# Kernel optimization log

Hardware: AMD Instinct MI355X
Metric: run time of the kernel (lower is better)

The kernel has to match this reference:

```python
import jax, jax.numpy as jnp
import numpy as np

# static config (matches init_kwargs and a standard 4-level FPN for ~800px input)
SPATIAL_SHAPES = ((100, 100), (50, 50), (25, 25), (13, 13))  # (H_l, W_l)
B, C, H, L, P = 2, 256, 8, 4, 4
DFFN = 2048
DH = C // H
LQ = sum(h * w for h, w in SPATIAL_SHAPES)  # 13294


def layer_norm(x, g, b, eps=1e-5):
    m = jnp.mean(x, -1, keepdims=True)
    v = jnp.mean((x - m) ** 2, -1, keepdims=True)
    return (x - m) * jax.lax.rsqrt(v + eps) * g + b


def ms_deform_sample(value, loc, attn):
    # value [B,Lv,H,DH], loc [B,Lq,H,L,P,2] in [0,1], attn [B,Lq,H,L,P]
    value = jnp.transpose(value, (0, 2, 1, 3))  # [B,H,Lv,DH]
    lq = loc.shape[1]
    out = jnp.zeros((B, H, lq, DH), value.dtype)
    start = 0
    for l, (Hl, Wl) in enumerate(SPATIAL_SHAPES):
        v = jax.lax.dynamic_slice_in_dim(value, start, Hl * Wl, axis=2)  # [B,H,N_l,DH]
        # grid_sample(align_corners=False) coords: x = loc_x*W - 0.5
        gx = jnp.transpose(loc[:, :, :, l, :, 0], (0, 2, 1, 3)) * Wl - 0.5  # [B,H,Lq,P]
        gy = jnp.transpose(loc[:, :, :, l, :, 1], (0, 2, 1, 3)) * Hl - 0.5
        aw = jnp.transpose(attn[:, :, :, l, :], (0, 2, 1, 3))  # [B,H,Lq,P]
        x0 = jnp.floor(gx)
        y0 = jnp.floor(gy)
        for dx in (0.0, 1.0):
            for dy in (0.0, 1.0):
                xi = x0 + dx
                yi = y0 + dy
                w = (1.0 - jnp.abs(gx - xi)) * (1.0 - jnp.abs(gy - yi))
                valid = (xi >= 0) & (xi < Wl) & (yi >= 0) & (yi < Hl)
                idx = (jnp.clip(yi, 0, Hl - 1) * Wl + jnp.clip(xi, 0, Wl - 1)).astype(jnp.int32)
                g = jnp.take_along_axis(v, idx.reshape(B, H, -1)[..., None], axis=2)  # [B,H,Lq*P,DH]
                ww = (w * aw * valid.astype(w.dtype))[..., None]  # [B,H,Lq,P,1]
                out = out + jnp.sum(g.reshape(B, H, lq, P, DH) * ww, axis=3)
        start += Hl * Wl
    return jnp.transpose(out, (0, 2, 1, 3)).reshape(B, lq, C)


def setup_inputs() -> dict:
    key = jax.random.key(0)
    ks = jax.random.split(key, 16)
    s = 0.02
    return {
        "src": jax.random.normal(ks[0], (B, LQ, C), jnp.float32),
        "pos": jax.random.normal(ks[1], (B, LQ, C), jnp.float32),
        "reference_points": jax.random.uniform(ks[2], (B, LQ, L, 2), jnp.float32),
        "w_value": jax.random.normal(ks[3], (C, C), jnp.float32) * s,
        "b_value": jnp.zeros((C,), jnp.float32),
        "w_off": jax.random.normal(ks[4], (C, H * L * P * 2), jnp.float32) * s,
        "b_off": jax.random.normal(ks[5], (H * L * P * 2,), jnp.float32) * s,
        "w_attn": jax.random.normal(ks[6], (C, H * L * P), jnp.float32) * s,
        "b_attn": jnp.zeros((H * L * P,), jnp.float32),
        "w_out": jax.random.normal(ks[7], (C, C), jnp.float32) * s,
        "b_out": jnp.zeros((C,), jnp.float32),
        "ln1_g": jnp.ones((C,), jnp.float32),
        "ln1_b": jnp.zeros((C,), jnp.float32),
        "w_ffn1": jax.random.normal(ks[8], (C, DFFN), jnp.float32) * s,
        "b_ffn1": jnp.zeros((DFFN,), jnp.float32),
        "w_ffn2": jax.random.normal(ks[9], (DFFN, C), jnp.float32) * s,
        "b_ffn2": jnp.zeros((C,), jnp.float32),
        "ln2_g": jnp.ones((C,), jnp.float32),
        "ln2_b": jnp.zeros((C,), jnp.float32),
    }


def reference(src, pos, reference_points, w_value, b_value, w_off, b_off, w_attn, b_attn,
              w_out, b_out, ln1_g, ln1_b, w_ffn1, b_ffn1, w_ffn2, b_ffn2, ln2_g, ln2_b):
    # DeformableTransformerEncoderLayer.forward (eval mode, no dropout)
    q = src + pos  # with_pos_embed
    lq = q.shape[1]
    value = (src @ w_value + b_value).reshape(B, -1, H, DH)
    off = (q @ w_off + b_off).reshape(B, lq, H, L, P, 2)
    attn = (q @ w_attn + b_attn).reshape(B, lq, H, L * P)
    attn = jax.nn.softmax(attn, axis=-1).reshape(B, lq, H, L, P)
    # offset_normalizer = (W_l, H_l)
    norm = jnp.array([[w, h] for h, w in SPATIAL_SHAPES], dtype=src.dtype)
    loc = reference_points[:, :, None, :, None, :] + off / norm[None, None, None, :, None, :]
    src2 = ms_deform_sample(value, loc, attn) @ w_out + b_out
    x = layer_norm(src + src2, ln1_g, ln1_b)
    ff = jax.nn.relu(x @ w_ffn1 + b_ffn1) @ w_ffn2 + b_ffn2
    return layer_norm(x + ff, ln2_g, ln2_b)
```

## Files before the change

### kernel.cpp

```cpp
#include <hip/hip_runtime.h>

#define LQN   13294
#define NBAT  2
#define MROWS (NBAT * LQN)
#define CCH   256
#define NHEAD 8
#define DHEAD 32
#define NLVL  4
#define NPT   4
#define DFF   2048

typedef short short8 __attribute__((ext_vector_type(8)));
typedef float f32x4 __attribute__((ext_vector_type(4)));
typedef unsigned short u16;
typedef u16 u16x4 __attribute__((ext_vector_type(4)));
typedef unsigned int u32;
typedef u32 u32x4 __attribute__((ext_vector_type(4)));

__device__ __forceinline__ u16 f2bf(float f) {
  unsigned int u = __builtin_bit_cast(unsigned int, f);
  u += 0x7fffu + ((u >> 16) & 1u);
  return (u16)(u >> 16);
}
__device__ __forceinline__ float bf2f(u16 s) {
  unsigned int u = ((unsigned int)s) << 16;
  return __builtin_bit_cast(float, u);
}
__device__ __forceinline__ void async16(const void* g, void* l) {
  __builtin_amdgcn_global_load_lds(
      (const __attribute__((address_space(1))) void*)g,
      (__attribute__((address_space(3))) void*)l, 16, 0, 0);
}

__global__ __launch_bounds__(256, 2)
void gemm_dual(const u16* __restrict__ A0, const u16* __restrict__ BT0,
               const float* __restrict__ bias0, u16* __restrict__ C0,
               const u16* __restrict__ A1, const u16* __restrict__ BT1,
               const float* __restrict__ bias1, u16* __restrict__ C1)
{
  __shared__ u16 As[2][128 * 64];
  __shared__ u16 Bs[2][128 * 64];
  const int t    = threadIdx.x;
  const int lane = t & 63;
  const int wid  = t >> 6;
  const int wm   = wid >> 1, wn = wid & 1;
  const int bm   = blockIdx.x;
  const int bnG  = blockIdx.y;
  const bool first = bnG < 2;
  const u16* A    = first ? A0 : A1;
  const u16* BT   = first ? BT0 : BT1;
  const float* bias = first ? bias0 : bias1;
  const int  bn   = first ? bnG : bnG - 2;
  const int l15  = lane & 15;
  const int kq   = lane >> 4;

  f32x4 acc[4][4];
#pragma unroll
  for (int m = 0; m < 4; ++m)
#pragma unroll
    for (int n = 0; n < 4; ++n) acc[m][n] = (f32x4)0.0f;

  auto stage = [&](int buf, int kt) {
#pragma unroll
    for (int i = 0; i < 4; ++i) {
      const int c   = i * 256 + t;
      const int row = c >> 3;
      const int kg  = (c & 7) ^ (row & 7);
      int ar = bm * 128 + row; ar = ar < MROWS ? ar : MROWS - 1;
      async16(&A[(size_t)ar * 256 + kt + kg * 8], &As[buf][c * 8]);
      const int br = bn * 128 + row;
      async16(&BT[(size_t)br * 256 + kt + kg * 8], &Bs[buf][c * 8]);
    }
  };

  stage(0, 0);
  __syncthreads();
  int cur = 0;

  for (int kt = 0; kt < 256; kt += 64) {
    if (kt + 64 < 256) stage(cur ^ 1, kt + 64);

#pragma unroll
    for (int kk = 0; kk < 2; ++kk) {
      short8 af[4], bfr[4];
#pragma unroll
      for (int m = 0; m < 4; ++m) {
        const int row = wm * 64 + m * 16 + l15;
        const int xb  = (kk * 64 + kq * 16) ^ ((row & 7) << 4);
        af[m] = *(const short8*)((const char*)&As[cur][0] + row * 128 + xb);
      }
#pragma unroll
      for (int n = 0; n < 4; ++n) {
        const int col = wn * 64 + n * 16 + l15;
        const int xb  = (kk * 64 + kq * 16) ^ ((col & 7) << 4);
        bfr[n] = *(const short8*)((const char*)&Bs[cur][0] + col * 128 + xb);
      }
#pragma unroll
      for (int m = 0; m < 4; ++m)
#pragma unroll
        for (int n = 0; n < 4; ++n)
          acc[m][n] = __builtin_amdgcn_mfma_f32_16x16x32_bf16(af[m], bfr[n], acc[m][n], 0, 0, 0);
    }

    __syncthreads();
    cur ^= 1;
  }

  const int crow0 = bm * 128 + wm * 64;
  const int ccol0 = bn * 128 + wn * 64;
#pragma unroll
  for (int n = 0; n < 4; ++n) {
    int col = ccol0 + n * 16 + l15;
    float bv = bias[col];
#pragma unroll
    for (int m = 0; m < 4; ++m) {
      int rbase = crow0 + m * 16 + kq * 4;
#pragma unroll
      for (int j = 0; j < 4; ++j) {
        int row = rbase + j;
        if (row < MROWS) {
          float v = acc[m][n][j] + bv;
          if (first) C0[(size_t)row * 256 + col] = f2bf(v);
          else       C1[(size_t)row * 384 + col] = f2bf(v);
        }
      }
    }
  }
}

__global__ __launch_bounds__(512, 2)
void outproj_ln1(const u16* __restrict__ src2_bf, const u16* __restrict__ WT_out,
                 const float* __restrict__ b_out, const float* __restrict__ src,
                 const float* __restrict__ g1, const float* __restrict__ be1,
                 u16* __restrict__ x_bf)
{
  extern __shared__ char smem[];
  char* As = smem;
  char* Bs = smem + 16384;
  float2* red = (float2*)(smem + 49152);

  const int t    = threadIdx.x;
  const int lane = t & 63;
  const int wid  = t >> 6;
  const int wm   = wid >> 2, wn = wid & 3;
  const int l15  = lane & 15;
  const int kq   = lane >> 4;
  const int bm   = blockIdx.x;

  auto stage = [&](int kt) {
#pragma unroll
    for (int i = 0; i < 2; ++i) {
      const int c   = i * 512 + t;
      const int row = c >> 3;
      const int kg  = (c & 7) ^ (row & 7);
      int ar = bm * 128 + row; ar = ar < MROWS ? ar : MROWS - 1;
      async16(&src2_bf[(size_t)ar * 256 + kt + kg * 8], As + c * 16);
    }
#pragma unroll
    for (int i = 0; i < 4; ++i) {
      const int c   = i * 512 + t;
      const int row = c >> 3;
      const int kg  = (c & 7) ^ (row & 7);
      async16(&WT_out[(size_t)row * 256 + kt + kg * 8], Bs + c * 16);
    }
  };

  f32x4 acc[4][4];
#pragma unroll
  for (int m = 0; m < 4; ++m)
#pragma unroll
    for (int n = 0; n < 4; ++n) acc[m][n] = (f32x4)0.0f;

  for (int kt = 0; kt < 256; kt += 64) {
    stage(kt);
    __syncthreads();

#pragma unroll
    for (int kk = 0; kk < 2; ++kk) {
      short8 af[4], bfr[4];
#pragma unroll
      for (int m = 0; m < 4; ++m) {
        const int row = wm * 64 + m * 16 + l15;
        const int xb  = (kk * 64 + kq * 16) ^ ((row & 7) << 4);
        af[m] = *(const short8*)(As + row * 128 + xb);
      }
#pragma unroll
      for (int n = 0; n < 4; ++n) {
        const int col = wn * 64 + n * 16 + l15;
        const int xb  = (kk * 64 + kq * 16) ^ ((col & 7) << 4);
        bfr[n] = *(const short8*)(Bs + col * 128 + xb);
      }
#pragma unroll
      for (int m = 0; m < 4; ++m)
#pragma unroll
        for (int n = 0; n < 4; ++n)
          acc[m][n] = __builtin_amdgcn_mfma_f32_16x16x32_bf16(af[m], bfr[n], acc[m][n], 0, 0, 0);
    }
    __syncthreads();
  }

#pragma unroll
  for (int n = 0; n < 4; ++n) {
    const int col = wn * 64 + n * 16 + l15;
    const float bv = b_out[col];
#pragma unroll
    for (int m = 0; m < 4; ++m)
#pragma unroll
      for (int j = 0; j < 4; ++j) {
        int row = bm * 128 + wm * 64 + m * 16 + kq * 4 + j;
        row = row < MROWS ? row : MROWS - 1;
        acc[m][n][j] += bv + src[(size_t)row * 256 + col];
      }
  }
  float s1[4][4], s2[4][4];
#pragma unroll
  for (int m = 0; m < 4; ++m)
#pragma unroll
    for (int j = 0; j < 4; ++j) {
      float a = 0.f, b = 0.f;
#pragma unroll
      for (int n = 0; n < 4; ++n) { const float v = acc[m][n][j]; a += v; b += v * v; }
      s1[m][j] = a; s2[m][j] = b;
    }
#pragma unroll
  for (int o = 1; o < 16; o <<= 1)
#pragma unroll
    for (int m = 0; m < 4; ++m)
#pragma unroll
      for (int j = 0; j < 4; ++j) {
        s1[m][j] += __shfl_xor(s1[m][j], o, 64);
        s2[m][j] += __shfl_xor(s2[m][j], o, 64);
      }
  if (l15 == 0)
#pragma unroll
    for (int m = 0; m < 4; ++m)
#pragma unroll
      for (int j = 0; j < 4; ++j)
        red[(wm * 64 + m * 16 + kq * 4 + j) * 4 + wn] = make_float2(s1[m][j], s2[m][j]);
  __syncthreads();
  float mean[4][4], rstd[4][4];
#pragma unroll
  for (int m = 0; m < 4; ++m)
#pragma unroll
    for (int j = 0; j < 4; ++j) {
      const int rl = wm * 64 + m * 16 + kq * 4 + j;
      float a = 0.f, b = 0.f;
#pragma unroll
      for (int w = 0; w < 4; ++w) { const float2 r = red[rl * 4 + w]; a += r.x; b += r.y; }
      const float mu = a * (1.0f / 256.0f);
      mean[m][j] = mu;
      rstd[m][j] = rsqrtf(b * (1.0f / 256.0f) - mu * mu + 1e-5f);
    }
#pragma unroll
  for (int n = 0; n < 4; ++n) {
    const int col = wn * 64 + n * 16 + l15;
    const float gg = g1[col], bb = be1[col];
#pragma unroll
    for (int m = 0; m < 4; ++m)
#pragma unroll
      for (int j = 0; j < 4; ++j) {
        const int row = bm * 128 + wm * 64 + m * 16 + kq * 4 + j;
        if (row < MROWS) {
          const float y = (acc[m][n][j] - mean[m][j]) * rstd[m][j] * gg + bb;
          x_bf[(size_t)row * 256 + col] = f2bf(y);
        }
      }
  }
}

__global__ __launch_bounds__(1024, 2)
void ffn_ln2(const u16* __restrict__ x_bf, const u16* __restrict__ W1T,
             const u16* __restrict__ W2T, const float* __restrict__ b1,
             const float* __restrict__ b2,
             const float* __restrict__ g2, const float* __restrict__ be2,
             float* __restrict__ out)
{
  extern __shared__ char smem[];
  u16*  w1s = (u16*)(smem);
  u16*  w2s = (u16*)(smem + 65536);
  char* ps  = smem + 131072;
  float2* red = (float2*)(smem + 149504);

  const int t    = threadIdx.x;
  const int lane = t & 63;
  const int wid  = t >> 6;
  const int l15  = lane & 15;
  const int kq   = lane >> 4;
  const int bm   = blockIdx.x;
  const int pwm  = wid >> 1, pwn = wid & 1;
  const int vwm  = wid >> 2, vwn = wid & 3;

  short8 xr[8];
  {
    int ar = bm * 128 + pwm * 16 + l15;
    ar = ar < MROWS ? ar : MROWS - 1;
    const char* xb = (const char*)x_bf + (size_t)ar * 512 + kq * 16;
#pragma unroll
    for (int ks = 0; ks < 8; ++ks) xr[ks] = *(const short8*)(xb + ks * 64);
  }

  auto stage = [&](int buf, int it) {
#pragma unroll
    for (int i = 0; i < 2; ++i) {
      const int c  = i * 1024 + t;
      const int r1 = c >> 5;
      const int k1 = ((c & 31) ^ (r1 & 7)) * 8;
      async16(&W1T[(size_t)(it * 64 + r1) * 256 + k1], &w1s[buf * 16384 + c * 8]);
      const int r2 = c >> 3;
      const int k2 = ((c & 7) ^ (r2 & 7)) * 8;
      async16(&W2T[(size_t)r2 * 2048 + it * 64 + k2], &w2s[buf * 16384 + c * 8]);
    }
  };

  f32x4 acc[2][4];
#pragma unroll
  for (int m = 0; m < 2; ++m)
#pragma unroll
    for (int n = 0; n < 4; ++n) acc[m][n] = (f32x4)0.0f;

  stage(0, 0);
  __syncthreads();

  for (int it = 0; it < 32; ++it) {
    const int cur = it & 1;
    if (it < 31) stage(cur ^ 1, it + 1);

    f32x4 p[2];
    p[0] = (f32x4)0.0f; p[1] = (f32x4)0.0f;
#pragma unroll
    for (int ks = 0; ks < 8; ++ks) {
#pragma unroll
      for (int n = 0; n < 2; ++n) {
        const int wrow = pwn * 32 + n * 16 + l15;
        const int xb   = (((ks * 4 + kq) ^ (wrow & 7)) << 4);
        const short8 bfr = *(const short8*)((const char*)&w1s[cur * 16384] + wrow * 512 + xb);
        p[n] = __builtin_amdgcn_mfma_f32_16x16x32_bf16(xr[ks], bfr, p[n], 0, 0, 0);
      }
    }

#pragma unroll
    for (int n = 0; n < 2; ++n) {
      const int col = pwn * 32 + n * 16 + l15;
      const float bv = b1[it * 64 + col];
#pragma unroll
      for (int j = 0; j < 4; ++j) {
        const int prow = pwm * 16 + kq * 4 + j;
        *(u16*)(ps + prow * 144 + col * 2) = f2bf(fmaxf(p[n][j] + bv, 0.0f));
      }
    }
    __syncthreads();

#pragma unroll
    for (int kk = 0; kk < 2; ++kk) {
      short8 paf[2];
#pragma unroll
      for (int m = 0; m < 2; ++m) {
        const int arow = vwm * 32 + m * 16 + l15;
        paf[m] = *(const short8*)(ps + arow * 144 + (kk * 4 + kq) * 16);
      }
#pragma unroll
      for (int n = 0; n < 4; ++n) {
        const int brow = vwn * 64 + n * 16 + l15;
        const int xb   = (((kk * 4 + kq) ^ (brow & 7)) << 4);
        const short8 bfr = *(const short8*)((const char*)&w2s[cur * 16384] + brow * 128 + xb);
#pragma unroll
        for (int m = 0; m < 2; ++m)
          acc[m][n] = __builtin_amdgcn_mfma_f32_16x16x32_bf16(paf[m], bfr, acc[m][n], 0, 0, 0);
      }
    }
    __syncthreads();
  }

#pragma unroll
  for (int n = 0; n < 4; ++n) {
    const int col = vwn * 64 + n * 16 + l15;
    const float bv = b2[col];
#pragma unroll
    for (int m = 0; m < 2; ++m)
#pragma unroll
      for (int j = 0; j < 4; ++j) {
        int row = bm * 128 + vwm * 32 + m * 16 + kq * 4 + j;
        row = row < MROWS ? row : MROWS - 1;
        acc[m][n][j] += bv + bf2f(x_bf[(size_t)row * 256 + col]);
      }
  }
  float s1[2][4], s2[2][4];
#pragma unroll
  for (int m = 0; m < 2; ++m)
#pragma unroll
    for (int j = 0; j < 4; ++j) {
      float a = 0.f, b = 0.f;
#pragma unroll
      for (int n = 0; n < 4; ++n) { const float v = acc[m][n][j]; a += v; b += v * v; }
      s1[m][j] = a; s2[m][j] = b;
    }
#pragma unroll
  for (int o = 1; o < 16; o <<= 1)
#pragma unroll
    for (int m = 0; m < 2; ++m)
#pragma unroll
      for (int j = 0; j < 4; ++j) {
        s1[m][j] += __shfl_xor(s1[m][j], o, 64);
        s2[m][j] += __shfl_xor(s2[m][j], o, 64);
      }
  if (l15 == 0)
#pragma unroll
    for (int m = 0; m < 2; ++m)
#pragma unroll
      for (int j = 0; j < 4; ++j)
        red[(vwm * 32 + m * 16 + kq * 4 + j) * 4 + vwn] = make_float2(s1[m][j], s2[m][j]);
  __syncthreads();
  float mean[2][4], rstd[2][4];
#pragma unroll
  for (int m = 0; m < 2; ++m)
#pragma unroll
    for (int j = 0; j < 4; ++j) {
      const int rl = vwm * 32 + m * 16 + kq * 4 + j;
      float a = 0.f, b = 0.f;
#pragma unroll
      for (int w = 0; w < 4; ++w) { const float2 r = red[rl * 4 + w]; a += r.x; b += r.y; }
      const float mu = a * (1.0f / 256.0f);
      mean[m][j] = mu;
      rstd[m][j] = rsqrtf(b * (1.0f / 256.0f) - mu * mu + 1e-5f);
    }
#pragma unroll
  for (int n = 0; n < 4; ++n) {
    const int col = vwn * 64 + n * 16 + l15;
    const float gg = g2[col], bb = be2[col];
#pragma unroll
    for (int m = 0; m < 2; ++m)
#pragma unroll
      for (int j = 0; j < 4; ++j) {
        const int row = bm * 128 + vwm * 32 + m * 16 + kq * 4 + j;
        if (row < MROWS)
          out[(size_t)row * 256 + col] = (acc[m][n][j] - mean[m][j]) * rstd[m][j] * gg + bb;
      }
  }
}

__global__ __launch_bounds__(256)
void sampler_kernel(const u16* __restrict__ offattn,
                    const float* __restrict__ refp,
                    const u16*  __restrict__ value,
                    u16*        __restrict__ src2)
{
  __shared__ float2 sWI[4][8][65];

  const int bid  = blockIdx.x;
  const int xcd  = bid & 7;
  const int idx  = bid >> 3;
  const int wg   = (xcd < 7) ? (xcd * 831 + idx) : (5817 + idx);

  const int t    = threadIdx.x;
  const int r4   = t >> 6;
  const int lane = t & 63;
  const int row  = wg * 4 + r4;
  const int b    = row / LQN;

  {
    const u16* oa = offattn + (size_t)row * 384;
    const float* rp = refp + (size_t)row * 8;
    const int p16 = lane & 15;
    const int l   = p16 >> 2;
    const int Wl  = (l == 0) ? 100 : (l == 1) ? 50 : (l == 2) ? 25 : 13;
    const int st  = (l == 0) ? 0 : (l == 1) ? 10000 : (l == 2) ? 12500 : 13125;
    const float rx = rp[l * 2 + 0] * (float)Wl - 0.5f;
    const float ry = rp[l * 2 + 1] * (float)Wl - 0.5f;

#pragma unroll
    for (int s = 0; s < 2; ++s) {
      const int h = s * 4 + (lane >> 4);
      float logit = bf2f(oa[256 + h * 16 + p16]);
      float mx = logit;
#pragma unroll
      for (int o = 1; o < 16; o <<= 1) mx = fmaxf(mx, __shfl_xor(mx, o, 64));
      float e = __expf(logit - mx);
      float ssum = e;
#pragma unroll
      for (int o = 1; o < 16; o <<= 1) ssum += __shfl_xor(ssum, o, 64);
      const float aw = e / ssum;

      const float ox = bf2f(oa[(h * 16 + p16) * 2 + 0]);
      const float oy = bf2f(oa[(h * 16 + p16) * 2 + 1]);
      const float gx = rx + ox;
      const float gy = ry + oy;
      const float x0f = floorf(gx), y0f = floorf(gy);
      const int   x0 = (int)x0f, y0 = (int)y0f;
      const float fx = gx - x0f, fy = gy - y0f;
#pragma unroll
      for (int c = 0; c < 4; ++c) {
        const int dx = c & 1, dy = c >> 1;
        const int xi = x0 + dx, yi = y0 + dy;
        const float wx = dx ? fx : 1.0f - fx;
        const float wy = dy ? fy : 1.0f - fy;
        const bool valid = (xi >= 0) && (xi < Wl) && (yi >= 0) && (yi < Wl);
        const int xc = min(max(xi, 0), Wl - 1);
        const int yc = min(max(yi, 0), Wl - 1);
        const int idxv = st + yc * Wl + xc;
        const float w = wx * wy * aw * (valid ? 1.0f : 0.0f);
        sWI[r4][h][p16 * 4 + c] = make_float2(w, __builtin_bit_cast(float, idxv));
      }
    }
  }
  __syncthreads();

  {
    const int e2 = lane >> 5;
    const int h  = (lane >> 2) & 7;
    const int c8 = lane & 3;
    const char* vbase = (const char*)value + (size_t)b * LQN * 512 + h * 64 + c8 * 16;
    const float2* wi = sWI[r4][h];

    float a[8];
#pragma unroll
    for (int i = 0; i < 8; ++i) a[i] = 0.f;

#pragma unroll 8
    for (int e = 0; e < 64; e += 2) {
      const float2 p = wi[e + e2];
      const float w  = p.x;
      const int  idxv = __builtin_bit_cast(int, p.y);
      const u32x4 u = *(const u32x4*)(vbase + (size_t)idxv * 512);
#pragma unroll
      for (int i = 0; i < 4; ++i) {
        a[2 * i]     += w * bf2f((u16)(u[i]));
        a[2 * i + 1] += w * bf2f((u16)(u[i] >> 16));
      }
    }
#pragma unroll
    for (int i = 0; i < 8; ++i) a[i] += __shfl_xor(a[i], 32, 64);

    if (e2 == 0) {
      u16 o[8];
#pragma unroll
      for (int i = 0; i < 8; ++i) o[i] = f2bf(a[i]);
      *(short8*)&src2[(size_t)row * 256 + h * 32 + c8 * 8] = *(short8*)o;
    }
  }
}

__global__ __launch_bounds__(256)
void prep_all(const float* __restrict__ src, const float* __restrict__ pos,
              u16* __restrict__ src_bf, u16* __restrict__ q_bf,
              const float* __restrict__ w_value, const float* __restrict__ w_off,
              const float* __restrict__ w_attn,  const float* __restrict__ w_out,
              const float* __restrict__ w_ffn1,  const float* __restrict__ w_ffn2,
              const float* __restrict__ b_off,   const float* __restrict__ b_attn,
              u16* __restrict__ WT_val, u16* __restrict__ WT_oa, u16* __restrict__ WT_out,
              u16* __restrict__ WT_f1,  u16* __restrict__ WT_f2, float* __restrict__ bias_oa)
{
  if (blockIdx.x < 6647) {
    const size_t i = (size_t)blockIdx.x * 256 + threadIdx.x;
    const f32x4 s = ((const f32x4*)src)[i];
    const f32x4 p = ((const f32x4*)pos)[i];
    u16x4 sb, qb;
#pragma unroll
    for (int j = 0; j < 4; ++j) { sb[j] = f2bf(s[j]); qb[j] = f2bf(s[j] + p[j]); }
    ((u16x4*)src_bf)[i] = sb;
    ((u16x4*)q_bf)[i]   = qb;
    return;
  }
  int i = (blockIdx.x - 6647) * 256 + threadIdx.x;
  if (i < 65536) {
    const int k = i >> 8, n = i & 255;
    WT_val[n * 256 + k] = f2bf(w_value[i]);
  } else if ((i -= 65536) < 65536) {
    const int k = i >> 8, n = i & 255;
    WT_oa[n * 256 + k] = f2bf(w_off[i]);
  } else if ((i -= 65536) < 32768) {
    const int k = i >> 7, n = i & 127;
    WT_oa[(256 + n) * 256 + k] = f2bf(w_attn[i]);
  } else if ((i -= 32768) < 65536) {
    const int k = i >> 8, n = i & 255;
    WT_out[n * 256 + k] = f2bf(w_out[i]);
  } else if ((i -= 65536) < 524288) {
    const int k = i >> 11, n = i & 2047;
    WT_f1[n * 256 + k] = f2bf(w_ffn1[i]);
  } else if ((i -= 524288) < 524288) {
    const int k = i >> 8, n = i & 255;
    WT_f2[n * 2048 + k] = f2bf(w_ffn2[i]);
  } else if ((i -= 524288) < 384) {
    bias_oa[i] = (i < 256) ? b_off[i] : b_attn[i - 256];
  }
}

extern "C" void kernel_launch(void* const* d_in, const int* in_sizes, int n_in,
                              void* d_out, int out_size, void* d_ws, size_t ws_size,
                              hipStream_t stream)
{
  const float* src     = (const float*)d_in[0];
  const float* pos     = (const float*)d_in[1];
  const float* refp    = (const float*)d_in[2];
  const float* w_value = (const float*)d_in[3];
  const float* b_value = (const float*)d_in[4];
  const float* w_off   = (const float*)d_in[5];
  const float* b_off   = (const float*)d_in[6];
  const float* w_attn  = (const float*)d_in[7];
  const float* b_attn  = (const float*)d_in[8];
  const float* w_out   = (const float*)d_in[9];
  const float* b_out   = (const float*)d_in[10];
  const float* ln1_g   = (const float*)d_in[11];
  const float* ln1_b   = (const float*)d_in[12];
  const float* w_ffn1  = (const float*)d_in[13];
  const float* b_ffn1  = (const float*)d_in[14];
  const float* w_ffn2  = (const float*)d_in[15];
  const float* b_ffn2  = (const float*)d_in[16];
  const float* ln2_g   = (const float*)d_in[17];
  const float* ln2_b   = (const float*)d_in[18];

  char* ws = (char*)d_ws;
  size_t off = 0;
  auto alloc = [&](size_t bytes) { void* p = ws + off; off += (bytes + 255) & ~(size_t)255; return p; };

  u16*   src_bf   = (u16*)  alloc((size_t)MROWS * 256 * 2);
  u16*   q_bf     = (u16*)  alloc((size_t)MROWS * 256 * 2);
  u16*   offattn  = (u16*)  alloc((size_t)MROWS * 384 * 2);
  u16*   value_bf = (u16*)  alloc((size_t)MROWS * 256 * 2);
  u16*   src2_bf  = (u16*)  alloc((size_t)MROWS * 256 * 2);
  u16*   WT_val   = (u16*)  alloc(256 * 256 * 2);
  u16*   WT_oa    = (u16*)  alloc(384 * 256 * 2);
  u16*   WT_out   = (u16*)  alloc(256 * 256 * 2);
  u16*   WT_f1    = (u16*)  alloc(2048 * 256 * 2);
  u16*   WT_f2    = (u16*)  alloc((size_t)256 * 2048 * 2);
  float* bias_oa  = (float*)alloc(384 * 4);

  u16* x_bf = q_bf;

  prep_all<<<6647 + 4994, 256, 0, stream>>>(src, pos, src_bf, q_bf,
                                            w_value, w_off, w_attn, w_out, w_ffn1, w_ffn2,
                                            b_off, b_attn,
                                            WT_val, WT_oa, WT_out, WT_f1, WT_f2, bias_oa);

  static bool attr_set = false;
  if (!attr_set) {
    hipFuncSetAttribute((const void*)ffn_ln2,
                        hipFuncAttributeMaxDynamicSharedMemorySize, 153600);
    hipFuncSetAttribute((const void*)outproj_ln1,
                        hipFuncAttributeMaxDynamicSharedMemorySize, 53248);
    attr_set = true;
  }

  gemm_dual<<<dim3(208, 5), 256, 0, stream>>>(src_bf, WT_val, b_value, value_bf,
                                              q_bf, WT_oa, bias_oa, offattn);

  sampler_kernel<<<MROWS / 4, 256, 0, stream>>>(offattn, refp, value_bf, src2_bf);

  outproj_ln1<<<208, 512, 53248, stream>>>(src2_bf, WT_out, b_out, src,
                                           ln1_g, ln1_b, x_bf);

  ffn_ln2<<<208, 1024, 153600, stream>>>(x_bf, WT_f1, WT_f2, b_ffn1, b_ffn2,
                                         ln2_g, ln2_b, (float*)d_out);
}
```

Measured before the change: 237.0 us.

## Load FFN2 weights directly to registers and halve FFN chunk with double-buffered P tile

The fused FFN kernel no longer stages W2 through LDS. Each wave loads its W2 fragments straight from global memory into registers. The hidden dimension is now processed in 64 chunks of 32 instead of 32 chunks of 64, with the intermediate ReLU tile double-buffered so only one barrier per iteration is needed. This shrinks LDS from 150KB to 56KB and cuts LDS traffic and barriers, at the cost of uncoalesced per-lane global reads of W2 and more iterations with smaller MFMA work per sync.

```diff
diff --git a/kernel.cpp b/kernel.cpp
--- a/kernel.cpp
+++ b/kernel.cpp
@@ -268,7 +268,7 @@
   }
 }
 
-__global__ __launch_bounds__(1024, 2)
+__global__ __launch_bounds__(1024)
 void ffn_ln2(const u16* __restrict__ x_bf, const u16* __restrict__ W1T,
              const u16* __restrict__ W2T, const float* __restrict__ b1,
              const float* __restrict__ b2,
@@ -276,10 +276,11 @@
              float* __restrict__ out)
 {
   extern __shared__ char smem[];
-  u16*  w1s = (u16*)(smem);
-  u16*  w2s = (u16*)(smem + 65536);
-  char* ps  = smem + 131072;
-  float2* red = (float2*)(smem + 149504);
+  char* w1s0 = smem;
+  char* w1s1 = smem + 16384;
+  char* ps0  = smem + 32768;
+  char* ps1  = smem + 43008;
+  float2* red = (float2*)(smem + 53248);
 
   const int t    = threadIdx.x;
   const int lane = t & 63;
@@ -299,17 +300,11 @@
     for (int ks = 0; ks < 8; ++ks) xr[ks] = *(const short8*)(xb + ks * 64);
   }
 
-  auto stage = [&](int buf, int it) {
-#pragma unroll
-    for (int i = 0; i < 2; ++i) {
-      const int c  = i * 1024 + t;
-      const int r1 = c >> 5;
-      const int k1 = ((c & 31) ^ (r1 & 7)) * 8;
-      async16(&W1T[(size_t)(it * 64 + r1) * 256 + k1], &w1s[buf * 16384 + c * 8]);
-      const int r2 = c >> 3;
-      const int k2 = ((c & 7) ^ (r2 & 7)) * 8;
-      async16(&W2T[(size_t)r2 * 2048 + it * 64 + k2], &w2s[buf * 16384 + c * 8]);
-    }
+  auto stage_w1 = [&](char* buf, int it) {
+    const int c  = t;
+    const int r1 = c >> 5;
+    const int k1 = ((c & 31) ^ (r1 & 7)) * 8;
+    async16(&W1T[(size_t)(it * 32 + r1) * 256 + k1], buf + c * 16);
   };
 
   f32x4 acc[2][4];
@@ -318,57 +313,54 @@
 #pragma unroll
     for (int n = 0; n < 4; ++n) acc[m][n] = (f32x4)0.0f;
 
-  stage(0, 0);
+  stage_w1(w1s0, 0);
   __syncthreads();
 
-  for (int it = 0; it < 32; ++it) {
-    const int cur = it & 1;
-    if (it < 31) stage(cur ^ 1, it + 1);
-
-    f32x4 p[2];
-    p[0] = (f32x4)0.0f; p[1] = (f32x4)0.0f;
-#pragma unroll
-    for (int ks = 0; ks < 8; ++ks) {
-#pragma unroll
-      for (int n = 0; n < 2; ++n) {
-        const int wrow = pwn * 32 + n * 16 + l15;
+  const u16* w2base = W2T + (size_t)(vwn * 64 + l15) * 2048 + kq * 8;
+
+  for (int it = 0; it < 64; ++it) {
+    short8 w2r[4];
+#pragma unroll
+    for (int n = 0; n < 4; ++n)
+      w2r[n] = *(const short8*)(w2base + (size_t)n * 16 * 2048 + it * 32);
+
+    if (it < 63) stage_w1((it & 1) ? w1s0 : w1s1, it + 1);
+
+    {
+      const char* w1u = (it & 1) ? w1s1 : w1s0;
+      char* psW = (it & 1) ? ps1 : ps0;
+      f32x4 p = (f32x4)0.0f;
+#pragma unroll
+      for (int ks = 0; ks < 8; ++ks) {
+        const int wrow = pwn * 16 + l15;
         const int xb   = (((ks * 4 + kq) ^ (wrow & 7)) << 4);
-        const short8 bfr = *(const short8*)((const char*)&w1s[cur * 16384] + wrow * 512 + xb);
-        p[n] = __builtin_amdgcn_mfma_f32_16x16x32_bf16(xr[ks], bfr, p[n], 0, 0, 0);
-      }
-    }
-
-#pragma unroll
-    for (int n = 0; n < 2; ++n) {
-      const int col = pwn * 32 + n * 16 + l15;
-      const float bv = b1[it * 64 + col];
+        const short8 bfr = *(const short8*)(w1u + wrow * 512 + xb);
+        p = __builtin_amdgcn_mfma_f32_16x16x32_bf16(xr[ks], bfr, p, 0, 0, 0);
+      }
+      const int col = pwn * 16 + l15;
+      const float bv = b1[it * 32 + col];
 #pragma unroll
       for (int j = 0; j < 4; ++j) {
         const int prow = pwm * 16 + kq * 4 + j;
-        *(u16*)(ps + prow * 144 + col * 2) = f2bf(fmaxf(p[n][j] + bv, 0.0f));
+        *(u16*)(psW + prow * 80 + col * 2) = f2bf(fmaxf(p[j] + bv, 0.0f));
       }
     }
     __syncthreads();
 
-#pragma unroll
-    for (int kk = 0; kk < 2; ++kk) {
+    {
+      const char* psR = (it & 1) ? ps1 : ps0;
       short8 paf[2];
 #pragma unroll
       for (int m = 0; m < 2; ++m) {
         const int arow = vwm * 32 + m * 16 + l15;
-        paf[m] = *(const short8*)(ps + arow * 144 + (kk * 4 + kq) * 16);
-      }
-#pragma unroll
-      for (int n = 0; n < 4; ++n) {
-        const int brow = vwn * 64 + n * 16 + l15;
-        const int xb   = (((kk * 4 + kq) ^ (brow & 7)) << 4);
-        const short8 bfr = *(const short8*)((const char*)&w2s[cur * 16384] + brow * 128 + xb);
+        paf[m] = *(const short8*)(psR + arow * 80 + kq * 16);
+      }
+#pragma unroll
+      for (int n = 0; n < 4; ++n)
 #pragma unroll
         for (int m = 0; m < 2; ++m)
-          acc[m][n] = __builtin_amdgcn_mfma_f32_16x16x32_bf16(paf[m], bfr, acc[m][n], 0, 0, 0);
-      }
-    }
-    __syncthreads();
+          acc[m][n] = __builtin_amdgcn_mfma_f32_16x16x32_bf16(paf[m], w2r[n], acc[m][n], 0, 0, 0);
+    }
   }
 
 #pragma unroll
@@ -403,6 +395,7 @@
         s1[m][j] += __shfl_xor(s1[m][j], o, 64);
         s2[m][j] += __shfl_xor(s2[m][j], o, 64);
       }
+  __syncthreads();
   if (l15 == 0)
 #pragma unroll
     for (int m = 0; m < 2; ++m)
@@ -634,7 +627,7 @@
   static bool attr_set = false;
   if (!attr_set) {
     hipFuncSetAttribute((const void*)ffn_ln2,
-                        hipFuncAttributeMaxDynamicSharedMemorySize, 153600);
+                        hipFuncAttributeMaxDynamicSharedMemorySize, 57344);
     hipFuncSetAttribute((const void*)outproj_ln1,
                         hipFuncAttributeMaxDynamicSharedMemorySize, 53248);
     attr_set = true;
@@ -648,6 +641,6 @@
   outproj_ln1<<<208, 512, 53248, stream>>>(src2_bf, WT_out, b_out, src,
                                            ln1_g, ln1_b, x_bf);
 
-  ffn_ln2<<<208, 1024, 153600, stream>>>(x_bf, WT_f1, WT_f2, b_ffn1, b_ffn2,
-                                         ln2_g, ln2_b, (float*)d_out);
-}
+  ffn_ln2<<<208, 1024, 57344, stream>>>(x_bf, WT_f1, WT_f2, b_ffn1, b_ffn2,
+                                        ln2_g, ln2_b, (float*)d_out);
+}
```

After: 319.8 us. +35.0%, slower.
